# Kernel optimization log

Hardware: AMD Instinct MI355X
Metric: run time of the kernel (lower is better)

Reference implementation:

```python
import jax, jax.numpy as jnp
import numpy as np

B, S, D, H = 4, 2048, 1024, 16
DK = D // H


def setup_inputs() -> dict:
    key = jax.random.key(0)
    ks = jax.random.split(key, 11)
    scale = 1.0 / np.sqrt(D)
    inp = {
        "query": jax.random.normal(ks[0], (B, S, D), jnp.float32),
        "key": jax.random.normal(ks[1], (B, S, D), jnp.float32),
        "value": jax.random.normal(ks[2], (B, S, D), jnp.float32),
    }
    # 4 linear layers: Wq, Wk, Wv, Wo (torch Linear: y = x @ W.T + b)
    for i, name in enumerate(["q", "k", "v", "o"]):
        inp[f"W{name}"] = jax.random.uniform(ks[3 + 2 * i], (D, D), jnp.float32, -scale, scale)
        inp[f"b{name}"] = jax.random.uniform(ks[4 + 2 * i], (D,), jnp.float32, -scale, scale)
    return inp


def reference(query, key, value, Wq, bq, Wk, bk, Wv, bv, Wo, bo):
    def proj(x, W, b):
        # [B,S,D] -> [B,H,S,DK]
        y = x @ W.T + b
        return y.reshape(B, S, H, DK).transpose(0, 2, 1, 3)

    q = proj(query, Wq, bq)
    k = proj(key, Wk, bk)
    v = proj(value, Wv, bv)
    scores = jnp.einsum("bhqd,bhkd->bhqk", q, k) / jnp.sqrt(jnp.float32(DK))
    p = jax.nn.softmax(scores, axis=-1)  # dropout p=0 -> identity
    ctx = jnp.einsum("bhqk,bhkd->bhqd", p, v)
    ctx = ctx.transpose(0, 2, 1, 3).reshape(B, S, D)
    return ctx @ Wo.T + bo
```

## Files before the change

### kernel.cpp

```cpp
#include <hip/hip_runtime.h>

typedef unsigned short u16;
typedef unsigned int u32;
typedef __attribute__((ext_vector_type(8))) short short8v;
typedef __attribute__((ext_vector_type(4))) short short4v;
typedef __attribute__((ext_vector_type(4))) float floatx4;

#define BB 4
#define SS 2048
#define DD 1024
#define HH 16
#define DKK 64
#define MM (BB * SS)
#define KK DD
#define NN DD
#define QSCALE 0.18033688011112042f

#define PS_RS 12
#define PS_CS 200
#define PS_REGION 1600

__device__ __forceinline__ u16 f2bf(float f) {
  union { __bf16 h; u16 u; } r; r.h = (__bf16)f; return r.u;
}
__device__ __forceinline__ u32 pack2bf(float a, float b) {
  union { u32 u; __bf16 h[2]; } r;
  r.h[0] = (__bf16)a; r.h[1] = (__bf16)b; return r.u;
}
__device__ __forceinline__ short8v cat44(short4v a, short4v b) {
  return __builtin_shufflevector(a, b, 0, 1, 2, 3, 4, 5, 6, 7);
}

__device__ __forceinline__ void load_lds16(const void* g, void* l) {
  __builtin_amdgcn_global_load_lds((const __attribute__((address_space(1))) void*)g,
                                   (__attribute__((address_space(3))) void*)l, 16, 0, 0);
}

__device__ __forceinline__ floatx4 mfma_k32(short8v a, short8v b, floatx4 c) {
  return __builtin_amdgcn_mfma_f32_16x16x32_bf16(a, b, c, 0, 0, 0);
}

__global__ __launch_bounds__(256) void cvt_w4(const float* __restrict__ w0,
                                              const float* __restrict__ w1,
                                              const float* __restrict__ w2,
                                              const float* __restrict__ w3,
                                              u16* __restrict__ out) {
  const int y = blockIdx.y;
  const float* in = (y == 0) ? w0 : (y == 1) ? w1 : (y == 2) ? w2 : w3;
  u16* o = out + (size_t)y * DD * DD;
  const int i = (blockIdx.x * 256 + threadIdx.x) * 8;
  float4 a = *(const float4*)(in + i);
  float4 b = *(const float4*)(in + i + 4);
  uint4 v;
  v.x = pack2bf(a.x, a.y); v.y = pack2bf(a.z, a.w);
  v.z = pack2bf(b.x, b.y); v.w = pack2bf(b.z, b.w);
  *(uint4*)(o + i) = v;
}

__global__ __launch_bounds__(256) void cvt_a3(const float* __restrict__ a0,
                                              const float* __restrict__ a1,
                                              const float* __restrict__ a2,
                                              u16* __restrict__ o0, u16* __restrict__ o1,
                                              u16* __restrict__ o2) {
  const int y = blockIdx.y;
  const float* in = (y == 0) ? a0 : (y == 1) ? a1 : a2;
  u16* o = (y == 0) ? o0 : (y == 1) ? o1 : o2;
  const int i = (blockIdx.x * 256 + threadIdx.x) * 8;
  float4 a = *(const float4*)(in + i);
  float4 b = *(const float4*)(in + i + 4);
  uint4 v;
  v.x = pack2bf(a.x, a.y); v.y = pack2bf(a.z, a.w);
  v.z = pack2bf(b.x, b.y); v.w = pack2bf(b.z, b.w);
  *(uint4*)(o + i) = v;
}

#define NT (KK / 64)
#define ITERS (NT / 2)

__device__ __forceinline__ void stage_half(const u16* __restrict__ gsrc, u16* ldst,
                                           int tid) {
#pragma unroll
  for (int L = 0; L < 2; ++L) {
    const int s = L * 512 + tid;
    const int r = s >> 3;
    const int g = (s & 7) ^ (r & 7);
    load_lds16(gsrc + (size_t)r * KK + g * 8, ldst + s * 8);
  }
}

__device__ __forceinline__ void gemm256_core(const u16* __restrict__ A,
                                             const u16* __restrict__ W,
                                             u16* As, u16* Bs,
                                             floatx4 (&acc)[8][4]) {
  const int tid = threadIdx.x;
  const int w = tid >> 6, lane = tid & 63;
  const int wm = w >> 2, wn = w & 3;
  const int wnh = wn >> 1, wno = wn & 1;
  const int lr = lane & 15;
  const int c0 = (((lane >> 2) & 1) << 5) | ((((lane >> 4) ^ lane) & 3) << 3);

#define AP(d, fr, kk) \
  (*(const short8v*)(As + ((d)*2 + wm) * 8192 + ((fr)*16 + lr) * 64 + (c0 ^ ((kk)*32))))
#define BP(d, fc, kk) \
  (*(const short8v*)(Bs + ((d)*2 + wnh) * 8192 + (wno * 64 + (fc)*16 + lr) * 64 + (c0 ^ ((kk)*32))))
#define MFMA8(FROFF, B, FCOFF)                                                  \
  _Pragma("unroll") for (int fr_ = 0; fr_ < 4; ++fr_)                           \
  _Pragma("unroll") for (int fc_ = 0; fc_ < 2; ++fc_) {                         \
    acc[(FROFF) + fr_][(FCOFF) + fc_] =                                         \
        mfma_k32(a[fr_][0], B[fc_][0], acc[(FROFF) + fr_][(FCOFF) + fc_]);      \
    acc[(FROFF) + fr_][(FCOFF) + fc_] =                                         \
        mfma_k32(a[fr_][1], B[fc_][1], acc[(FROFF) + fr_][(FCOFF) + fc_]);      \
  }
#define BAR() __builtin_amdgcn_s_barrier()
#define PRIO1() __builtin_amdgcn_s_setprio(1)
#define PRIO0() __builtin_amdgcn_s_setprio(0)

  short8v a[4][2], b01[2][2], b23[2][2];

  stage_half(A, As + 0 * 8192, tid);
  stage_half(A + (size_t)128 * KK, As + 1 * 8192, tid);
  stage_half(W, Bs + 0 * 8192, tid);
  stage_half(W + (size_t)128 * KK, Bs + 1 * 8192, tid);
  stage_half(W + 64, Bs + 2 * 8192, tid);
  stage_half(W + (size_t)128 * KK + 64, Bs + 3 * 8192, tid);
  asm volatile("s_waitcnt vmcnt(4)" ::: "memory");
  BAR();

#pragma unroll 1
  for (int j = 0; j < ITERS; ++j) {
    const int e = 2 * j, o = e + 1;
    const bool haveE2 = (j + 1 < ITERS);
#pragma unroll
    for (int fr = 0; fr < 4; ++fr) { a[fr][0] = AP(0, fr, 0); a[fr][1] = AP(0, fr, 1); }
#pragma unroll
    for (int fc = 0; fc < 2; ++fc) { b01[fc][0] = BP(0, fc, 0); b01[fc][1] = BP(0, fc, 1); }
    stage_half(A + (size_t)o * 64, As + 2 * 8192, tid);
    BAR(); PRIO1(); MFMA8(0, b01, 0); PRIO0(); BAR();
#pragma unroll
    for (int fc = 0; fc < 2; ++fc) { b23[fc][0] = BP(0, fc + 2, 0); b23[fc][1] = BP(0, fc + 2, 1); }
    stage_half(A + (size_t)128 * KK + (size_t)o * 64, As + 3 * 8192, tid);
    BAR(); PRIO1(); MFMA8(0, b23, 2); PRIO0(); BAR();
#pragma unroll
    for (int fr = 0; fr < 4; ++fr) { a[fr][0] = AP(0, fr + 4, 0); a[fr][1] = AP(0, fr + 4, 1); }
    if (haveE2) stage_half(W + (size_t)(e + 2) * 64, Bs + 0 * 8192, tid);
    BAR(); PRIO1(); MFMA8(4, b01, 0); PRIO0(); BAR();
    if (haveE2) {
      stage_half(W + (size_t)128 * KK + (size_t)(e + 2) * 64, Bs + 1 * 8192, tid);
      asm volatile("s_waitcnt vmcnt(4)" ::: "memory");
    } else {
      asm volatile("s_waitcnt vmcnt(0)" ::: "memory");
    }
    BAR(); PRIO1(); MFMA8(4, b23, 2); PRIO0(); BAR();
#pragma unroll
    for (int fr = 0; fr < 4; ++fr) { a[fr][0] = AP(1, fr, 0); a[fr][1] = AP(1, fr, 1); }
#pragma unroll
    for (int fc = 0; fc < 2; ++fc) { b01[fc][0] = BP(1, fc, 0); b01[fc][1] = BP(1, fc, 1); }
    if (haveE2) stage_half(A + (size_t)(e + 2) * 64, As + 0 * 8192, tid);
    BAR(); PRIO1(); MFMA8(0, b01, 0); PRIO0(); BAR();
#pragma unroll
    for (int fc = 0; fc < 2; ++fc) { b23[fc][0] = BP(1, fc + 2, 0); b23[fc][1] = BP(1, fc + 2, 1); }
    if (haveE2) stage_half(A + (size_t)128 * KK + (size_t)(e + 2) * 64, As + 1 * 8192, tid);
    BAR(); PRIO1(); MFMA8(0, b23, 2); PRIO0(); BAR();
#pragma unroll
    for (int fr = 0; fr < 4; ++fr) { a[fr][0] = AP(1, fr + 4, 0); a[fr][1] = AP(1, fr + 4, 1); }
    if (haveE2) stage_half(W + (size_t)(o + 2) * 64, Bs + 2 * 8192, tid);
    BAR(); PRIO1(); MFMA8(4, b01, 0); PRIO0(); BAR();
    if (haveE2) {
      stage_half(W + (size_t)128 * KK + (size_t)(o + 2) * 64, Bs + 3 * 8192, tid);
      asm volatile("s_waitcnt vmcnt(4)" ::: "memory");
    }
    BAR(); PRIO1(); MFMA8(4, b23, 2); PRIO0(); BAR();
  }
#undef AP
#undef BP
#undef MFMA8
#undef BAR
#undef PRIO1
#undef PRIO0
}

__global__ __launch_bounds__(512, 2) void proj_gemm(
    const u16* __restrict__ qc, const u16* __restrict__ kc, const u16* __restrict__ vc,
    const u16* __restrict__ Wq, const u16* __restrict__ Wk, const u16* __restrict__ Wv,
    const float* __restrict__ bq, const float* __restrict__ bk, const float* __restrict__ bv,
    u16* __restrict__ Qb, u16* __restrict__ Kb, u16* __restrict__ Vtb) {
  __shared__ __align__(16) u16 As[2 * 2 * 8192];
  __shared__ __align__(16) u16 Bs[2 * 2 * 8192];
  const int z = blockIdx.z;
  const u16* A = (z == 0) ? qc : (z == 1) ? kc : vc;
  const u16* W = (z == 0) ? Wq : (z == 1) ? Wk : Wv;
  const float* bias = (z == 0) ? bq : (z == 1) ? bk : bv;
  const int m0 = blockIdx.x * 256, n0 = blockIdx.y * 256;

  floatx4 acc[8][4] = {};
  gemm256_core(A + (size_t)m0 * KK, W + (size_t)n0 * KK, As, Bs, acc);

  const int tid = threadIdx.x;
  const int w = tid >> 6, lane = tid & 63;
  const int lr = lane & 15, lq = lane >> 4;
  const int wm = w >> 2, wn = w & 3;
  const int row0 = m0 + wm * 128;
  const int col0 = n0 + wn * 64;

  if (z == 2) {
#pragma unroll
    for (int fc = 0; fc < 4; ++fc) {
      const int col = col0 + fc * 16 + lr;
      const float bv_ = bias[col];
      const int h = col >> 6, dk = col & 63;
#pragma unroll
      for (int fr = 0; fr < 8; ++fr) {
        const int row = row0 + fr * 16 + lq * 4;
        const int b = row >> 11, s = row & (SS - 1);
        uint2 pk;
        pk.x = pack2bf(acc[fr][fc][0] + bv_, acc[fr][fc][1] + bv_);
        pk.y = pack2bf(acc[fr][fc][2] + bv_, acc[fr][fc][3] + bv_);
        *(uint2*)&Vtb[(((size_t)(b * HH + h)) * DKK + dk) * SS + s] = pk;
      }
    }
  } else {
    u16* out = (z == 0) ? Qb : Kb;
    const float sc = (z == 0) ? QSCALE : 1.0f;
#pragma unroll
    for (int fc = 0; fc < 4; ++fc) {
      const int col = col0 + fc * 16 + lr;
      const float bv_ = bias[col];
#pragma unroll
      for (int fr = 0; fr < 8; ++fr)
#pragma unroll
        for (int rr = 0; rr < 4; ++rr) {
          const int row = row0 + fr * 16 + lq * 4 + rr;
          out[(size_t)row * NN + col] = f2bf((acc[fr][fc][rr] + bv_) * sc);
        }
    }
  }
}

__global__ __launch_bounds__(512, 2) void out_gemm(const u16* __restrict__ A,
                                                   const u16* __restrict__ W,
                                                   const float* __restrict__ bias,
                                                   float* __restrict__ out) {
  __shared__ __align__(16) u16 As[2 * 2 * 8192];
  __shared__ __align__(16) u16 Bs[2 * 2 * 8192];
  const int m0 = blockIdx.x * 256, n0 = blockIdx.y * 256;
  floatx4 acc[8][4] = {};
  gemm256_core(A + (size_t)m0 * KK, W + (size_t)n0 * KK, As, Bs, acc);

  const int tid = threadIdx.x;
  const int w = tid >> 6, lane = tid & 63;
  const int lr = lane & 15, lq = lane >> 4;
  const int wm = w >> 2, wn = w & 3;
  const int row0 = m0 + wm * 128;
  const int col0 = n0 + wn * 64;
#pragma unroll
  for (int fc = 0; fc < 4; ++fc) {
    const int col = col0 + fc * 16 + lr;
    const float bv = bias[col];
#pragma unroll
    for (int fr = 0; fr < 8; ++fr)
#pragma unroll
      for (int rr = 0; rr < 4; ++rr) {
        const int row = row0 + fr * 16 + lq * 4 + rr;
        out[(size_t)row * NN + col] = acc[fr][fc][rr] + bv;
      }
  }
}

__global__ __launch_bounds__(256, 4) void attn_kernel(const u16* __restrict__ Q,
                                                      const u16* __restrict__ Kmat,
                                                      const u16* __restrict__ Vt,
                                                      u16* __restrict__ ctx) {
  __shared__ __align__(16) u16 Ks[2][64 * 64];
  __shared__ __align__(16) u16 Vs[64 * 64];
  __shared__ __align__(16) u16 Ps[4 * PS_REGION];
  const int tid = threadIdx.x;
  const int w = tid >> 6, lane = tid & 63;
  const int lr = lane & 15, lq = lane >> 4;
  const int bh = blockIdx.x, b = bh >> 4, h = bh & 15;
  const int q0 = blockIdx.y * 128;

  short8v qf[2][2];
  {
    const u16* qp = Q + ((size_t)(b * SS + q0 + w * 32 + lr)) * DD + h * 64 + lq * 8;
    qf[0][0] = *(const short8v*)qp;
    qf[0][1] = *(const short8v*)(qp + 32);
    qf[1][0] = *(const short8v*)(qp + 16 * DD);
    qf[1][1] = *(const short8v*)(qp + 16 * DD + 32);
  }
  floatx4 o[2][4] = {};
  float l_part[2][4] = {};

  const u16* kp = Kmat + ((size_t)(b * SS + w * 16 + lr)) * DD + h * 64 + lq * 8;
  const u16* vp = Vt + (((size_t)(b * HH + h)) * DKK + w * 16 + lr) * SS + lq * 8;

  load_lds16(kp,      &Ks[0][(2 * w) * 512]);
  load_lds16(kp + 32, &Ks[0][(2 * w + 1) * 512]);
  kp += 64 * DD;

#pragma unroll 1
  for (int kt = 0; kt < SS / 64; ++kt) {
    const int bf = kt & 1;
    const bool haveNext = (kt + 1 < SS / 64);
    __builtin_amdgcn_s_barrier();
    load_lds16(vp,      &Vs[(2 * w) * 512]);
    load_lds16(vp + 32, &Vs[(2 * w + 1) * 512]);
    vp += 64;
    if (haveNext) {
      load_lds16(kp,      &Ks[bf ^ 1][(2 * w) * 512]);
      load_lds16(kp + 32, &Ks[bf ^ 1][(2 * w + 1) * 512]);
      kp += 64 * DD;
      asm volatile("s_waitcnt vmcnt(4)" ::: "memory");
    } else {
      asm volatile("s_waitcnt vmcnt(2)" ::: "memory");
    }
    __builtin_amdgcn_s_barrier();

    floatx4 sc[2][4] = {};
    __builtin_amdgcn_s_setprio(1);
#pragma unroll
    for (int t = 0; t < 4; ++t) {
      short8v kb0 = *(const short8v*)&Ks[bf][t * 1024 + lane * 8];
      short8v kb1 = *(const short8v*)&Ks[bf][t * 1024 + 512 + lane * 8];
#pragma unroll
      for (int s = 0; s < 2; ++s) {
        sc[s][t] = mfma_k32(qf[s][0], kb0, sc[s][t]);
        sc[s][t] = mfma_k32(qf[s][1], kb1, sc[s][t]);
      }
    }
    __builtin_amdgcn_s_setprio(0);

    short8v pa[2][2];
#pragma unroll
    for (int s = 0; s < 2; ++s) {
#pragma unroll
      for (int t = 0; t < 4; ++t) {
#pragma unroll
        for (int r = 0; r < 4; ++r) {
          const float e = __builtin_amdgcn_exp2f(sc[s][t][r]);
          sc[s][t][r] = e;
          l_part[s][r] += e;
        }
      }
      u16* pw = &Ps[w * PS_REGION];
#pragma unroll
      for (int t = 0; t < 4; ++t) {
        const int base = (2 * t + (lr >> 3)) * PS_CS + (lr & 7);
#pragma unroll
        for (int r = 0; r < 4; ++r)
          pw[base + (lq * 4 + r) * PS_RS] = f2bf(sc[s][t][r]);
      }
      {
        const u16* rp0 = pw + lq * PS_CS + lr * PS_RS;
        const u16* rp1 = pw + (4 + lq) * PS_CS + lr * PS_RS;
        pa[s][0] = cat44(*(const short4v*)rp0, *(const short4v*)(rp0 + 4));
        pa[s][1] = cat44(*(const short4v*)rp1, *(const short4v*)(rp1 + 4));
      }
    }

    if (haveNext) {
      asm volatile("s_waitcnt vmcnt(2)" ::: "memory");
    } else {
      asm volatile("s_waitcnt vmcnt(0)" ::: "memory");
    }
    __builtin_amdgcn_s_barrier();

    __builtin_amdgcn_s_setprio(1);
#pragma unroll
    for (int t = 0; t < 4; ++t) {
      short8v vb0 = *(const short8v*)&Vs[t * 1024 + lane * 8];
      short8v vb1 = *(const short8v*)&Vs[t * 1024 + 512 + lane * 8];
#pragma unroll
      for (int s = 0; s < 2; ++s) {
        o[s][t] = mfma_k32(pa[s][0], vb0, o[s][t]);
        o[s][t] = mfma_k32(pa[s][1], vb1, o[s][t]);
      }
    }
    __builtin_amdgcn_s_setprio(0);
  }

  float inv[2][4];
#pragma unroll
  for (int s = 0; s < 2; ++s)
#pragma unroll
    for (int r = 0; r < 4; ++r) {
      float l = l_part[s][r];
      l += __shfl_xor(l, 1); l += __shfl_xor(l, 2);
      l += __shfl_xor(l, 4); l += __shfl_xor(l, 8);
      inv[s][r] = 1.0f / l;
    }

#pragma unroll
  for (int s = 0; s < 2; ++s)
#pragma unroll
    for (int r = 0; r < 4; ++r) {
      const int sq = q0 + w * 32 + s * 16 + lq * 4 + r;
      u16* cp = ctx + ((size_t)(b * SS + sq)) * DD + h * 64;
      const float iv = inv[s][r];
#pragma unroll
      for (int t = 0; t < 4; ++t)
        cp[t * 16 + lr] = f2bf(o[s][t][r] * iv);
    }
}

extern "C" void kernel_launch(void* const* d_in, const int* in_sizes, int n_in,
                              void* d_out, int out_size, void* d_ws, size_t ws_size,
                              hipStream_t stream) {
  const float* query = (const float*)d_in[0];
  const float* key   = (const float*)d_in[1];
  const float* value = (const float*)d_in[2];
  const float* Wq = (const float*)d_in[3];  const float* bq = (const float*)d_in[4];
  const float* Wk = (const float*)d_in[5];  const float* bk = (const float*)d_in[6];
  const float* Wv = (const float*)d_in[7];  const float* bv = (const float*)d_in[8];
  const float* Wo = (const float*)d_in[9];  const float* bo = (const float*)d_in[10];
  float* out = (float*)d_out;

  char* ws = (char*)d_ws;
  size_t off = 0;
  u16* Wb   = (u16*)(ws + off); off += (size_t)4 * DD * DD * 2;
  u16* Qb   = (u16*)(ws + off); off += (size_t)MM * DD * 2;
  u16* Kb   = (u16*)(ws + off); off += (size_t)MM * DD * 2;
  u16* Vtb  = (u16*)(ws + off); off += (size_t)MM * DD * 2;
  u16* qc   = (u16*)(ws + off);
  u16* ctxb = qc;               off += (size_t)MM * DD * 2;
  u16* kc = (u16*)d_out;
  u16* vc = (u16*)d_out + (size_t)MM * DD;
  u16* Wq_b = Wb, *Wk_b = Wb + (size_t)DD * DD, *Wv_b = Wb + (size_t)2 * DD * DD,
     *Wo_b = Wb + (size_t)3 * DD * DD;

  const int wn = DD * DD, an = MM * DD;
  cvt_w4<<<dim3(wn / 2048, 4), 256, 0, stream>>>(Wq, Wk, Wv, Wo, Wb);
  cvt_a3<<<dim3(an / 2048, 3), 256, 0, stream>>>(query, key, value, qc, kc, vc);

  proj_gemm<<<dim3(MM / 256, NN / 256, 3), 512, 0, stream>>>(
      qc, kc, vc, Wq_b, Wk_b, Wv_b, bq, bk, bv, Qb, Kb, Vtb);

  attn_kernel<<<dim3(BB * HH, SS / 128), 256, 0, stream>>>(Qb, Kb, Vtb, ctxb);

  out_gemm<<<dim3(MM / 256, NN / 256), 512, 0, stream>>>(ctxb, Wo_b, bo, out);
}
```

Before: 342.1 us.

## Keep P in registers via transposed QK^T MFMA and double-buffer V tiles

```diff
diff --git a/kernel.cpp b/kernel.cpp
--- a/kernel.cpp
+++ b/kernel.cpp
@@ -15,10 +15,6 @@
 #define KK DD
 #define NN DD
 #define QSCALE 0.18033688011112042f
-
-#define PS_RS 12
-#define PS_CS 200
-#define PS_REGION 1600
 
 __device__ __forceinline__ u16 f2bf(float f) {
   union { __bf16 h; u16 u; } r; r.h = (__bf16)f; return r.u;
@@ -266,13 +262,12 @@
   }
 }
 
-__global__ __launch_bounds__(256, 4) void attn_kernel(const u16* __restrict__ Q,
+__global__ __launch_bounds__(256, 5) void attn_kernel(const u16* __restrict__ Q,
                                                       const u16* __restrict__ Kmat,
                                                       const u16* __restrict__ Vt,
                                                       u16* __restrict__ ctx) {
   __shared__ __align__(16) u16 Ks[2][64 * 64];
-  __shared__ __align__(16) u16 Vs[64 * 64];
-  __shared__ __align__(16) u16 Ps[4 * PS_REGION];
+  __shared__ __align__(16) u16 Vs[2][64 * 64];
   const int tid = threadIdx.x;
   const int w = tid >> 6, lane = tid & 63;
   const int lr = lane & 15, lq = lane >> 4;
@@ -288,30 +283,32 @@
     qf[1][1] = *(const short8v*)(qp + 16 * DD + 32);
   }
   floatx4 o[2][4] = {};
-  float l_part[2][4] = {};
+  float l_part[2] = {};
 
   const u16* kp = Kmat + ((size_t)(b * SS + w * 16 + lr)) * DD + h * 64 + lq * 8;
   const u16* vp = Vt + (((size_t)(b * HH + h)) * DKK + w * 16 + lr) * SS + lq * 8;
+  const int vbase = 128 * (lq >> 1) + 8 * lr + 4 * (lq & 1);
 
   load_lds16(kp,      &Ks[0][(2 * w) * 512]);
   load_lds16(kp + 32, &Ks[0][(2 * w + 1) * 512]);
-  kp += 64 * DD;
+  load_lds16(vp,      &Vs[0][(2 * w) * 512]);
+  load_lds16(vp + 32, &Vs[0][(2 * w + 1) * 512]);
+  kp += 64 * DD; vp += 64;
 
 #pragma unroll 1
   for (int kt = 0; kt < SS / 64; ++kt) {
     const int bf = kt & 1;
     const bool haveNext = (kt + 1 < SS / 64);
     __builtin_amdgcn_s_barrier();
-    load_lds16(vp,      &Vs[(2 * w) * 512]);
-    load_lds16(vp + 32, &Vs[(2 * w + 1) * 512]);
-    vp += 64;
     if (haveNext) {
       load_lds16(kp,      &Ks[bf ^ 1][(2 * w) * 512]);
       load_lds16(kp + 32, &Ks[bf ^ 1][(2 * w + 1) * 512]);
-      kp += 64 * DD;
+      load_lds16(vp,      &Vs[bf ^ 1][(2 * w) * 512]);
+      load_lds16(vp + 32, &Vs[bf ^ 1][(2 * w + 1) * 512]);
+      kp += 64 * DD; vp += 64;
       asm volatile("s_waitcnt vmcnt(4)" ::: "memory");
     } else {
-      asm volatile("s_waitcnt vmcnt(2)" ::: "memory");
+      asm volatile("s_waitcnt vmcnt(0)" ::: "memory");
     }
     __builtin_amdgcn_s_barrier();
 
@@ -323,8 +320,8 @@
       short8v kb1 = *(const short8v*)&Ks[bf][t * 1024 + 512 + lane * 8];
 #pragma unroll
       for (int s = 0; s < 2; ++s) {
-        sc[s][t] = mfma_k32(qf[s][0], kb0, sc[s][t]);
-        sc[s][t] = mfma_k32(qf[s][1], kb1, sc[s][t]);
+        sc[s][t] = mfma_k32(kb0, qf[s][0], sc[s][t]);
+        sc[s][t] = mfma_k32(kb1, qf[s][1], sc[s][t]);
       }
     }
     __builtin_amdgcn_s_setprio(0);
@@ -332,43 +329,35 @@
     short8v pa[2][2];
 #pragma unroll
     for (int s = 0; s < 2; ++s) {
-#pragma unroll
-      for (int t = 0; t < 4; ++t) {
+      float lp = 0.0f;
+#pragma unroll
+      for (int t = 0; t < 4; ++t)
 #pragma unroll
         for (int r = 0; r < 4; ++r) {
           const float e = __builtin_amdgcn_exp2f(sc[s][t][r]);
           sc[s][t][r] = e;
-          l_part[s][r] += e;
+          lp += e;
         }
+      l_part[s] += lp;
+#pragma unroll
+      for (int H = 0; H < 2; ++H) {
+        union { u32 u[4]; short8v v; } pb;
+        pb.u[0] = pack2bf(sc[s][2 * H][0], sc[s][2 * H][1]);
+        pb.u[1] = pack2bf(sc[s][2 * H][2], sc[s][2 * H][3]);
+        pb.u[2] = pack2bf(sc[s][2 * H + 1][0], sc[s][2 * H + 1][1]);
+        pb.u[3] = pack2bf(sc[s][2 * H + 1][2], sc[s][2 * H + 1][3]);
+        pa[s][H] = pb.v;
       }
-      u16* pw = &Ps[w * PS_REGION];
-#pragma unroll
-      for (int t = 0; t < 4; ++t) {
-        const int base = (2 * t + (lr >> 3)) * PS_CS + (lr & 7);
-#pragma unroll
-        for (int r = 0; r < 4; ++r)
-          pw[base + (lq * 4 + r) * PS_RS] = f2bf(sc[s][t][r]);
-      }
-      {
-        const u16* rp0 = pw + lq * PS_CS + lr * PS_RS;
-        const u16* rp1 = pw + (4 + lq) * PS_CS + lr * PS_RS;
-        pa[s][0] = cat44(*(const short4v*)rp0, *(const short4v*)(rp0 + 4));
-        pa[s][1] = cat44(*(const short4v*)rp1, *(const short4v*)(rp1 + 4));
-      }
-    }
-
-    if (haveNext) {
-      asm volatile("s_waitcnt vmcnt(2)" ::: "memory");
-    } else {
-      asm volatile("s_waitcnt vmcnt(0)" ::: "memory");
-    }
-    __builtin_amdgcn_s_barrier();
-
+    }
+
+    const u16* vsb = &Vs[bf][0];
     __builtin_amdgcn_s_setprio(1);
 #pragma unroll
     for (int t = 0; t < 4; ++t) {
-      short8v vb0 = *(const short8v*)&Vs[t * 1024 + lane * 8];
-      short8v vb1 = *(const short8v*)&Vs[t * 1024 + 512 + lane * 8];
+      short8v vb0 = cat44(*(const short4v*)&vsb[t * 1024 + vbase],
+                          *(const short4v*)&vsb[t * 1024 + vbase + 256]);
+      short8v vb1 = cat44(*(const short4v*)&vsb[t * 1024 + 512 + vbase],
+                          *(const short4v*)&vsb[t * 1024 + 512 + vbase + 256]);
 #pragma unroll
       for (int s = 0; s < 2; ++s) {
         o[s][t] = mfma_k32(pa[s][0], vb0, o[s][t]);
@@ -380,14 +369,14 @@
 
   float inv[2][4];
 #pragma unroll
-  for (int s = 0; s < 2; ++s)
-#pragma unroll
-    for (int r = 0; r < 4; ++r) {
-      float l = l_part[s][r];
-      l += __shfl_xor(l, 1); l += __shfl_xor(l, 2);
-      l += __shfl_xor(l, 4); l += __shfl_xor(l, 8);
-      inv[s][r] = 1.0f / l;
-    }
+  for (int s = 0; s < 2; ++s) {
+    float l = l_part[s];
+    l += __shfl_xor(l, 16);
+    l += __shfl_xor(l, 32);
+#pragma unroll
+    for (int r = 0; r < 4; ++r)
+      inv[s][r] = 1.0f / __shfl(l, lq * 4 + r);
+  }
 
 #pragma unroll
   for (int s = 0; s < 2; ++s)
```

After: 391.9 us. +14.5%, slower.
